# Optimization experiments

Hardware: AMD Instinct MI355X
Metric: run time of the kernel (lower is better)

Reference implementation:

```python
import jax, jax.numpy as jnp
import numpy as np

N = 5000      # nodes per event (hardcoded in PFNet7.forward)
BIN = 100     # LSH bin_size
K = 16        # kNN per node within bin
SLOPE = 0.01  # LeakyReLU default negative slope


def _mlp(x, W1, b1, W2, b2, W3, b3):
    h = jax.nn.leaky_relu(x @ W1 + b1, SLOPE)
    h = jax.nn.leaky_relu(h @ W2 + b2, SLOPE)
    return h @ W3 + b3


def _build_graph_lsh(x, codebook):
    # x: [N, F]. Faithful vectorized version of GraphBuildingLSH (batch=1).
    n_bins = N // BIN                                   # 50
    mul = x @ codebook[:, : n_bins // 2]                # [N, 25]
    cmul = jnp.concatenate([mul, -mul], axis=-1)        # [N, 50]
    bin_idx = jnp.argmax(cmul, axis=-1)                 # [N]
    bins_split = jnp.argsort(bin_idx).reshape(n_bins, BIN)  # [nb, BIN]
    pts = x[bins_split]                                 # [nb, BIN, F]
    dm = jax.nn.sigmoid(jnp.einsum('pif,pjf->pij', pts, pts))  # [nb, BIN, BIN]
    vals, inds = jax.lax.top_k(dm, K)                   # [nb, BIN, K]
    src = jnp.broadcast_to(bins_split[:, :, None], inds.shape).reshape(-1)
    dst = jnp.take_along_axis(bins_split, inds.reshape(n_bins, -1), axis=1).reshape(-1)
    val = vals.reshape(-1)                              # [nb*BIN*K] = 80000 edges
    return src, dst, val


def _gcn_conv(x, W, b, src, dst, ew):
    # PyG GCNConv: add self-loops (weight 1), symmetric normalization, aggregate at col.
    n = x.shape[0]
    loop = jnp.arange(n)
    row = jnp.concatenate([src, loop])
    col = jnp.concatenate([dst, loop])
    w = jnp.concatenate([ew, jnp.ones((n,), x.dtype)])
    deg = jax.ops.segment_sum(w, col, num_segments=n)
    dis = jnp.where(deg > 0, deg ** -0.5, 0.0)
    norm = dis[row] * w * dis[col]
    h = x @ W
    out = jax.ops.segment_sum(norm[:, None] * h[row], col, num_segments=n)
    return out + b


def _graph_conv(x, Wrel, brel, Wroot, src, dst, ew):
    # PyG GraphConv(aggr='add'): lin_rel(sum_j w_ij x_j) + lin_root(x)
    agg = jax.ops.segment_sum(ew[:, None] * x[src], dst, num_segments=x.shape[0])
    return agg @ Wrel + brel + x @ Wroot


def setup_inputs() -> dict:
    key = jax.random.key(0)
    ks = jax.random.split(key, 24)
    f32 = jnp.float32
    d = {
        'x': jax.random.normal(ks[0], (N, 12), f32),
        'ygen_id': jax.random.normal(ks[1], (N, 6), f32),
        'ygen': jax.random.normal(ks[2], (N, 6), f32),
        'codebook': jax.random.normal(ks[3], (12, 100), f32),
        # nn1: 12 -> 125 -> 125 -> 12
        'nn1_W1': jax.random.normal(ks[4], (12, 125), f32) * 0.1,
        'nn1_b1': jnp.zeros((125,), f32),
        'nn1_W2': jax.random.normal(ks[5], (125, 125), f32) * 0.1,
        'nn1_b2': jnp.zeros((125,), f32),
        'nn1_W3': jax.random.normal(ks[6], (125, 12), f32) * 0.1,
        'nn1_b3': jnp.zeros((12,), f32),
        # GCNConv: 12 -> 32
        'gcn_W': jax.random.normal(ks[7], (12, 32), f32) * 0.1,
        'gcn_b': jnp.zeros((32,), f32),
        # GraphConv: 32 -> 32
        'gc_Wrel': jax.random.normal(ks[8], (32, 32), f32) * 0.1,
        'gc_brel': jnp.zeros((32,), f32),
        'gc_Wroot': jax.random.normal(ks[9], (32, 32), f32) * 0.1,
        # nn2: 32 -> 125 -> 125 -> 6
        'nn2_W1': jax.random.normal(ks[10], (32, 125), f32) * 0.1,
        'nn2_b1': jnp.zeros((125,), f32),
        'nn2_W2': jax.random.normal(ks[11], (125, 125), f32) * 0.1,
        'nn2_b2': jnp.zeros((125,), f32),
        'nn2_W3': jax.random.normal(ks[12], (125, 6), f32) * 0.1,
        'nn2_b3': jnp.zeros((6,), f32),
        # nn3: 38 -> 125 -> 125 -> 6
        'nn3_W1': jax.random.normal(ks[13], (38, 125), f32) * 0.1,
        'nn3_b1': jnp.zeros((125,), f32),
        'nn3_W2': jax.random.normal(ks[14], (125, 125), f32) * 0.1,
        'nn3_b2': jnp.zeros((125,), f32),
        'nn3_W3': jax.random.normal(ks[15], (125, 6), f32) * 0.1,
        'nn3_b3': jnp.zeros((6,), f32),
    }
    return d


def reference(x, ygen_id, ygen, codebook,
              nn1_W1, nn1_b1, nn1_W2, nn1_b2, nn1_W3, nn1_b3,
              gcn_W, gcn_b, gc_Wrel, gc_brel, gc_Wroot,
              nn2_W1, nn2_b1, nn2_W2, nn2_b2, nn2_W3, nn2_b3,
              nn3_W1, nn3_b1, nn3_W2, nn3_b2, nn3_W3, nn3_b3):
    h = _mlp(x, nn1_W1, nn1_b1, nn1_W2, nn1_b2, nn1_W3, nn1_b3)   # [N, 12]
    src, dst, ew = _build_graph_lsh(h, codebook)
    h = jax.nn.leaky_relu(h, SLOPE)
    h = _gcn_conv(h, gcn_W, gcn_b, src, dst, ew)                   # [N, 32]
    h = _graph_conv(h, gc_Wrel, gc_brel, gc_Wroot, src, dst, ew)
    h = jax.nn.leaky_relu(h, SLOPE)
    cand_ids = _mlp(h, nn2_W1, nn2_b1, nn2_W2, nn2_b2, nn2_W3, nn2_b3)
    cand_p4 = _mlp(jnp.concatenate([h, cand_ids], axis=-1),
                   nn3_W1, nn3_b1, nn3_W2, nn3_b2, nn3_W3, nn3_b3)
    return (cand_ids, cand_p4, ygen_id, ygen)
```

## Files before the change

### kernel.cpp

```cpp
#include <hip/hip_runtime.h>
#include <math.h>

#define NN 5000
#define NBINS 50
#define BINSZ 100
#define KNN 16
#define BPAD 104
#define MROWS 112
#define NB 20

typedef _Float16 half8 __attribute__((ext_vector_type(8)));

__device__ __forceinline__ float lrelu(float x){ return x >= 0.f ? x : 0.01f*x; }

__global__ __launch_bounds__(640) void nn1_kernel(
    const float* __restrict__ x,
    const float* __restrict__ W1, const float* __restrict__ b1,
    const float* __restrict__ W2, const float* __restrict__ b2,
    const float* __restrict__ W3, const float* __restrict__ b3,
    const float* __restrict__ cb,
    float* __restrict__ h_out, int* __restrict__ bin_idx) {
    __shared__ float sW[8000];
    __shared__ float bufX[12 * NB];
    __shared__ float bufA[125 * NB];
    __shared__ float bufB[125 * NB];
    __shared__ float sCB[300];
    int tid = threadIdx.x;
    int n0 = blockIdx.x * NB;
    int g = tid >> 7, j = tid & 127;
    float acc[4];
    float4 r0, r1; float rt = 0.f;

    if (tid < 60) {
        float4 v = ((const float4*)(x + n0 * 12))[tid];
        int e = tid * 4;
        bufX[(e % 12) * NB + (e / 12)] = v.x;
        bufX[((e + 1) % 12) * NB + ((e + 1) / 12)] = v.y;
        bufX[((e + 2) % 12) * NB + ((e + 2) / 12)] = v.z;
        bufX[((e + 3) % 12) * NB + ((e + 3) / 12)] = v.w;
    }
    if (tid < 300) { int k = tid / 25, c = tid - k * 25; sCB[tid] = cb[k * 100 + c]; }
    if (tid < 375) ((float4*)sW)[tid] = ((const float4*)W1)[tid];
    __syncthreads();

    if (j < 125) {
        float bj = b1[j];
        acc[0] = bj; acc[1] = bj; acc[2] = bj; acc[3] = bj;
        #pragma unroll
        for (int k = 0; k < 12; ++k) {
            float w = sW[k * 125 + j];
            float4 a = *(const float4*)&bufX[k * NB + g * 4];
            acc[0] += a.x * w; acc[1] += a.y * w; acc[2] += a.z * w; acc[3] += a.w * w;
        }
        #pragma unroll
        for (int n = 0; n < 4; ++n) bufA[j * NB + g * 4 + n] = lrelu(acc[n]);
    }
    r0 = (tid < 1000) ? ((const float4*)W2)[tid] : make_float4(0.f,0.f,0.f,0.f);
    r1 = (tid < 360)  ? ((const float4*)W2)[tid + 640] : make_float4(0.f,0.f,0.f,0.f);
    __syncthreads();
    if (tid < 1000) ((float4*)sW)[tid] = r0;
    if (tid < 360)  ((float4*)sW)[tid + 640] = r1;
    __syncthreads();

    if (j < 125) { float bj = b2[j]; acc[0] = bj; acc[1] = bj; acc[2] = bj; acc[3] = bj; }
    for (int c = 0; c < 4; ++c) {
        if (c < 3) {
            int base = (c + 1) * 1000, nf4 = (c + 1 < 3) ? 1000 : 906;
            r0 = (tid < nf4) ? ((const float4*)W2)[base + tid] : make_float4(0.f,0.f,0.f,0.f);
            r1 = (tid + 640 < nf4) ? ((const float4*)W2)[base + tid + 640] : make_float4(0.f,0.f,0.f,0.f);
            if (c + 1 == 3 && tid == 0) rt = W2[15624];
        }
        int nk = (c < 3) ? 32 : 29;
        const float* wbuf = sW + (c & 1) * 4000;
        if (j < 125) {
            const float* arow = &bufA[(c * 32) * NB + g * 4];
            for (int k = 0; k < nk; ++k) {
                float w = wbuf[k * 125 + j];
                float4 a = *(const float4*)&arow[k * NB];
                acc[0] += a.x * w; acc[1] += a.y * w; acc[2] += a.z * w; acc[3] += a.w * w;
            }
        }
        if (c < 3) {
            float* dst = sW + ((c + 1) & 1) * 4000;
            int nf4 = (c + 1 < 3) ? 1000 : 906;
            if (tid < nf4) ((float4*)dst)[tid] = r0;
            if (tid + 640 < nf4) ((float4*)dst)[tid + 640] = r1;
            if (c + 1 == 3 && tid == 0) dst[3624] = rt;
            __syncthreads();
        }
    }
    if (j < 125) {
        #pragma unroll
        for (int n = 0; n < 4; ++n) bufB[j * NB + g * 4 + n] = lrelu(acc[n]);
    }
    __syncthreads();
    if (tid < 375) ((float4*)sW)[tid] = ((const float4*)W3)[tid];
    __syncthreads();

    if (j < 48) {
        int jj = j % 12, s = j / 12;
        int k0 = s * 32, nk = (s < 3) ? 32 : 29;
        float ps[4] = {0.f, 0.f, 0.f, 0.f};
        for (int k = 0; k < nk; ++k) {
            float w = sW[(k0 + k) * 12 + jj];
            float4 a = *(const float4*)&bufB[(k0 + k) * NB + g * 4];
            ps[0] += a.x * w; ps[1] += a.y * w; ps[2] += a.z * w; ps[3] += a.w * w;
        }
        #pragma unroll
        for (int n = 0; n < 4; ++n) bufA[(s * 12 + jj) * NB + g * 4 + n] = ps[n];
    }
    __syncthreads();
    if (tid < 240) {
        int jj = tid / 20, n = tid % 20;
        float v = bufA[jj * NB + n] + bufA[(12 + jj) * NB + n]
                + bufA[(24 + jj) * NB + n] + bufA[(36 + jj) * NB + n] + b3[jj];
        h_out[(n0 + n) * 12 + jj] = v;
        bufB[jj * NB + n] = v;
    }
    __syncthreads();

    if (tid < NB) {
        int n = tid;
        float hv[12];
        #pragma unroll
        for (int k = 0; k < 12; ++k) hv[k] = bufB[k * NB + n];
        float best = -INFINITY; int bi = 0;
        for (int c = 0; c < 25; ++c) {
            float m = 0.f;
            #pragma unroll
            for (int k = 0; k < 12; ++k) m += hv[k] * sCB[k * 25 + c];
            if (m > best) { best = m; bi = c; }
        }
        for (int c = 0; c < 25; ++c) {
            float m = 0.f;
            #pragma unroll
            for (int k = 0; k < 12; ++k) m += hv[k] * sCB[k * 25 + c];
            if (-m > best) { best = -m; bi = c + 25; }
        }
        bin_idx[n0 + n] = bi;
    }
}

__global__ __launch_bounds__(64) void scatter_kernel(
    const int* __restrict__ bin_idx, int* __restrict__ order) {
    __shared__ int sBI[NN];
    int b = blockIdx.x, lane = threadIdx.x;
    for (int t = lane; t < NN / 4; t += 64) ((int4*)sBI)[t] = ((const int4*)bin_idx)[t];
    __syncthreads();
    unsigned long long below = (lane == 0) ? 0ULL : ((~0ULL) >> (64 - lane));
    int cnt_lt = 0;
    for (int base = 0; base < NN; base += 64) {
        int i = base + lane;
        int bi = (i < NN) ? sBI[i] : 999;
        cnt_lt += __popcll(__ballot(bi < b));
    }
    int offs = cnt_lt;
    for (int base = 0; base < NN; base += 64) {
        int i = base + lane;
        int bi = (i < NN) ? sBI[i] : 999;
        unsigned long long m = __ballot(bi == b);
        if (bi == b) order[offs + __popcll(m & below)] = i;
        offs += __popcll(m);
    }
}

__global__ __launch_bounds__(256) void build_kernel(
    const float* __restrict__ h, const int* __restrict__ order,
    _Float16* __restrict__ Mg, float* __restrict__ dis_g) {
    __shared__ _Float16 M[BINSZ * BPAD];
    __shared__ float s_h[BINSZ * 12];
    __shared__ int   s_nodes[BINSZ];
    __shared__ unsigned s_tv[200 * KNN];
    int p = blockIdx.x, tid = threadIdx.x;

    if (tid < BINSZ) s_nodes[tid] = order[p * BINSZ + tid];
    for (int t = tid; t < BINSZ * BPAD / 2; t += 256) ((int*)M)[t] = 0;
    __syncthreads();
    for (int t = tid; t < BINSZ * 12; t += 256) {
        int i = t / 12, k = t - i * 12;
        s_h[t] = h[s_nodes[i] * 12 + k];
    }
    __syncthreads();

    if (tid < 200) {
        int row = tid >> 1, half = tid & 1;
        const float4* xp = (const float4*)&s_h[row * 12];
        float4 x0 = xp[0], x1 = xp[1], x2 = xp[2];
        unsigned tv[KNN];
        #pragma unroll
        for (int k = 0; k < KNN; ++k) tv[k] = 0u;
        int j0 = half * 50;
        for (int jj = 0; jj < 50; ++jj) {
            int j = j0 + jj;
            const float4* ap = (const float4*)&s_h[j * 12];
            float4 a0 = ap[0], a1 = ap[1], a2 = ap[2];
            float d = x0.x*a0.x + x0.y*a0.y + x0.z*a0.z + x0.w*a0.w
                    + x1.x*a1.x + x1.y*a1.y + x1.z*a1.z + x1.w*a1.w
                    + x2.x*a2.x + x2.y*a2.y + x2.z*a2.z + x2.w*a2.w;
            float v = 1.f / (1.f + expf(-d));
            unsigned key = (__float_as_uint(v) & 0xFFFFFF80u) | (unsigned)(127 - j);
            if (key > tv[KNN - 1]) {
                unsigned ins = key;
                #pragma unroll
                for (int k = 0; k < KNN; ++k) {
                    bool gt = ins > tv[k];
                    unsigned mx = gt ? ins : tv[k];
                    unsigned mn = gt ? tv[k] : ins;
                    tv[k] = mx; ins = mn;
                }
            }
        }
        #pragma unroll
        for (int k = 0; k < KNN; ++k) s_tv[tid * KNN + k] = tv[k];
    }
    __syncthreads();

    if (tid < BINSZ) {
        int base = tid * 32;
        int ia = 0, ib = 0;
        #pragma unroll
        for (int k = 0; k < KNN; ++k) {
            unsigned av = s_tv[base + ia], bv = s_tv[base + 16 + ib];
            bool tA = av > bv;
            unsigned key = tA ? av : bv;
            ia += tA; ib += !tA;
            int ix = 127 - (int)(key & 127u);
            float v = __uint_as_float(key & 0xFFFFFF80u);
            M[ix * BPAD + tid] = (_Float16)v;
        }
    }
    __syncthreads();

    for (int t = tid; t < BINSZ * BPAD / 8; t += 256)
        ((uint4*)(Mg + (size_t)p * BINSZ * BPAD))[t] = ((const uint4*)M)[t];
    if (tid < BINSZ) {
        float dsum = 1.0f;
        #pragma unroll 13
        for (int sc = 0; sc < 13; ++sc) {
            half8 m = *(const half8*)&M[tid * BPAD + sc * 8];
            dsum += (float)m[0] + (float)m[1] + (float)m[2] + (float)m[3]
                  + (float)m[4] + (float)m[5] + (float)m[6] + (float)m[7];
        }
        dis_g[p * BINSZ + tid] = 1.0f / sqrtf(dsum);
    }
}

__global__ __launch_bounds__(128) void conv_kernel(
    const _Float16* __restrict__ Mg, const float* __restrict__ dis_g,
    const float* __restrict__ h, const int* __restrict__ order,
    const float* __restrict__ gcn_W, const float* __restrict__ gcn_b,
    float* __restrict__ gcn_n, float* __restrict__ agg_n,
    const float4* __restrict__ ygen_id4, const float4* __restrict__ ygen4,
    float4* __restrict__ out4) {
    __shared__ _Float16 M[MROWS * BPAD];
    __shared__ float s_h[BINSZ * 12];
    __shared__ int   s_nodes[BINSZ];
    __shared__ float s_dis[BINSZ];
    __shared__ float s_w[12 * 8];
    __shared__ float s_hWd[8 * BPAD];
    __shared__ float s_gcn[8 * BPAD];
    int bid = blockIdx.x, tid = threadIdx.x;
    int p = bid >> 2, cg = bid & 3, c0 = cg * 8;

    if (tid < 75) {
        int gI = bid * 75 + tid;
        out4[15000 + gI] = (gI < 7500) ? ygen_id4[gI] : ygen4[gI - 7500];
    }
    if (tid < BINSZ) {
        s_nodes[tid] = order[p * BINSZ + tid];
        s_dis[tid]   = dis_g[p * BINSZ + tid];
    }
    for (int t = tid; t < 96; t += 128)
        s_w[t] = gcn_W[(t >> 3) * 32 + c0 + (t & 7)];
    for (int t = tid; t < BINSZ * BPAD / 8; t += 128)
        ((uint4*)M)[t] = ((const uint4*)(Mg + (size_t)p * BINSZ * BPAD))[t];
    for (int t = tid; t < (MROWS - BINSZ) * BPAD / 2; t += 128)
        ((int*)(M + BINSZ * BPAD))[t] = 0;
    if (tid < 32) {
        s_hWd[(tid >> 2) * BPAD + 100 + (tid & 3)] = 0.f;
        s_gcn[(tid >> 2) * BPAD + 100 + (tid & 3)] = 0.f;
    }
    __syncthreads();
    for (int t = tid; t < BINSZ * 12; t += 128) {
        int i = t / 12, k = t - i * 12;
        s_h[t] = h[s_nodes[i] * 12 + k];
    }
    __syncthreads();

    for (int o = tid; o < BINSZ * 8; o += 128) {
        int s = o >> 3, cc = o & 7;
        float a = 0.f;
        #pragma unroll
        for (int k = 0; k < 12; ++k) a += lrelu(s_h[s * 12 + k]) * s_w[k * 8 + cc];
        s_hWd[cc * BPAD + s] = s_dis[s] * a;
    }
    __syncthreads();

    int cc = tid & 7, dg = tid >> 3;
    {
        float acc[7];
        #pragma unroll
        for (int r = 0; r < 7; ++r) acc[r] = 0.f;
        for (int sc = 0; sc < 13; ++sc) {
            float4 hv0 = *(const float4*)&s_hWd[cc * BPAD + sc * 8];
            float4 hv1 = *(const float4*)&s_hWd[cc * BPAD + sc * 8 + 4];
            #pragma unroll
            for (int r = 0; r < 7; ++r) {
                int d = dg + 16 * r;
                half8 m = *(const half8*)&M[d * BPAD + sc * 8];
                acc[r] += (float)m[0]*hv0.x + (float)m[1]*hv0.y + (float)m[2]*hv0.z + (float)m[3]*hv0.w
                        + (float)m[4]*hv1.x + (float)m[5]*hv1.y + (float)m[6]*hv1.z + (float)m[7]*hv1.w;
            }
        }
        float bc = gcn_b[c0 + cc];
        #pragma unroll
        for (int r = 0; r < 7; ++r) {
            int d = dg + 16 * r;
            if (d < BINSZ) {
                float gq = s_dis[d] * (acc[r] + s_hWd[cc * BPAD + d]) + bc;
                s_gcn[cc * BPAD + d] = gq;
                gcn_n[s_nodes[d] * 32 + c0 + cc] = gq;
            }
        }
    }
    __syncthreads();
    {
        float acc[7];
        #pragma unroll
        for (int r = 0; r < 7; ++r) acc[r] = 0.f;
        for (int sc = 0; sc < 13; ++sc) {
            float4 hv0 = *(const float4*)&s_gcn[cc * BPAD + sc * 8];
            float4 hv1 = *(const float4*)&s_gcn[cc * BPAD + sc * 8 + 4];
            #pragma unroll
            for (int r = 0; r < 7; ++r) {
                int d = dg + 16 * r;
                half8 m = *(const half8*)&M[d * BPAD + sc * 8];
                acc[r] += (float)m[0]*hv0.x + (float)m[1]*hv0.y + (float)m[2]*hv0.z + (float)m[3]*hv0.w
                        + (float)m[4]*hv1.x + (float)m[5]*hv1.y + (float)m[6]*hv1.z + (float)m[7]*hv1.w;
            }
        }
        #pragma unroll
        for (int r = 0; r < 7; ++r) {
            int d = dg + 16 * r;
            if (d < BINSZ) agg_n[s_nodes[d] * 32 + c0 + cc] = acc[r];
        }
    }
}

__global__ __launch_bounds__(640) void nn23_kernel(
    const float* __restrict__ gcn_n, const float* __restrict__ agg_n,
    const float* __restrict__ Wrel, const float* __restrict__ brel,
    const float* __restrict__ Wroot,
    const float* __restrict__ A1, const float* __restrict__ ab1,
    const float* __restrict__ A2, const float* __restrict__ ab2,
    const float* __restrict__ A3, const float* __restrict__ ab3,
    const float* __restrict__ B1, const float* __restrict__ bb1,
    const float* __restrict__ B2, const float* __restrict__ bb2,
    const float* __restrict__ B3, const float* __restrict__ bb3,
    float* __restrict__ out_ids, float* __restrict__ out_p4) {
    __shared__ float sW[8000];
    __shared__ float sAG[32 * NB];
    __shared__ float sGC[32 * NB];
    __shared__ float bufC[38 * NB];
    __shared__ float bufA[125 * NB];
    __shared__ float bufB[125 * NB];
    int tid = threadIdx.x;
    int n0 = blockIdx.x * NB;
    int g = tid >> 7, j = tid & 127;
    float acc[4];
    float4 r0, r1; float rt = 0.f;

    if (tid < 160) {
        float4 va = ((const float4*)(agg_n + n0 * 32))[tid];
        float4 vg = ((const float4*)(gcn_n + n0 * 32))[tid];
        int e = tid * 4, n = e / 32, k = e % 32;
        sAG[k * NB + n] = va.x; sAG[(k+1) * NB + n] = va.y;
        sAG[(k+2) * NB + n] = va.z; sAG[(k+3) * NB + n] = va.w;
        sGC[k * NB + n] = vg.x; sGC[(k+1) * NB + n] = vg.y;
        sGC[(k+2) * NB + n] = vg.z; sGC[(k+3) * NB + n] = vg.w;
    }
    if (tid >= 160 && tid < 416) ((float4*)sW)[tid - 160] = ((const float4*)Wrel)[tid - 160];
    if (tid >= 416 && tid < 640) ((float4*)(sW + 1024))[tid - 416] = ((const float4*)Wroot)[tid - 416];
    if (tid < 32) ((float4*)(sW + 1024))[224 + tid] = ((const float4*)Wroot)[224 + tid];
    for (int t = tid; t < 1000; t += 640) ((float4*)(sW + 2048))[t] = ((const float4*)A1)[t];
    __syncthreads();

    {
        int jc = tid / 20, n = tid % 20;
        float a = brel[jc];
        #pragma unroll 8
        for (int k = 0; k < 32; ++k)
            a += sAG[k * NB + n] * sW[k * 32 + jc] + sGC[k * NB + n] * sW[1024 + k * 32 + jc];
        bufC[jc * NB + n] = lrelu(a);
    }
    __syncthreads();

    if (j < 125) {
        float bj = ab1[j];
        acc[0] = bj; acc[1] = bj; acc[2] = bj; acc[3] = bj;
        #pragma unroll 8
        for (int k = 0; k < 32; ++k) {
            float w = sW[2048 + k * 125 + j];
            float4 a = *(const float4*)&bufC[k * NB + g * 4];
            acc[0] += a.x * w; acc[1] += a.y * w; acc[2] += a.z * w; acc[3] += a.w * w;
        }
        #pragma unroll
        for (int n = 0; n < 4; ++n) bufA[j * NB + g * 4 + n] = lrelu(acc[n]);
    }
    r0 = (tid < 1000) ? ((const float4*)A2)[tid] : make_float4(0.f,0.f,0.f,0.f);
    r1 = (tid < 360)  ? ((const float4*)A2)[tid + 640] : make_float4(0.f,0.f,0.f,0.f);
    __syncthreads();
    if (tid < 1000) ((float4*)sW)[tid] = r0;
    if (tid < 360)  ((float4*)sW)[tid + 640] = r1;
    __syncthreads();

    if (j < 125) { float bj = ab2[j]; acc[0] = bj; acc[1] = bj; acc[2] = bj; acc[3] = bj; }
    for (int c = 0; c < 4; ++c) {
        if (c < 3) {
            int base = (c + 1) * 1000, nf4 = (c + 1 < 3) ? 1000 : 906;
            r0 = (tid < nf4) ? ((const float4*)A2)[base + tid] : make_float4(0.f,0.f,0.f,0.f);
            r1 = (tid + 640 < nf4) ? ((const float4*)A2)[base + tid + 640] : make_float4(0.f,0.f,0.f,0.f);
            if (c + 1 == 3 && tid == 0) rt = A2[15624];
        }
        int nk = (c < 3) ? 32 : 29;
        const float* wbuf = sW + (c & 1) * 4000;
        if (j < 125) {
            const float* arow = &bufA[(c * 32) * NB + g * 4];
            for (int k = 0; k < nk; ++k) {
                float w = wbuf[k * 125 + j];
                float4 a = *(const float4*)&arow[k * NB];
                acc[0] += a.x * w; acc[1] += a.y * w; acc[2] += a.z * w; acc[3] += a.w * w;
            }
        }
        if (c < 3) {
            float* dst = sW + ((c + 1) & 1) * 4000;
            int nf4 = (c + 1 < 3) ? 1000 : 906;
            if (tid < nf4) ((float4*)dst)[tid] = r0;
            if (tid + 640 < nf4) ((float4*)dst)[tid + 640] = r1;
            if (c + 1 == 3 && tid == 0) dst[3624] = rt;
            __syncthreads();
        }
    }
    if (j < 125) {
        #pragma unroll
        for (int n = 0; n < 4; ++n) bufB[j * NB + g * 4 + n] = lrelu(acc[n]);
    }
    __syncthreads();
    if (tid < 187) ((float4*)sW)[tid] = ((const float4*)A3)[tid];
    if (tid == 187) { sW[748] = A3[748]; sW[749] = A3[749]; }
    for (int t = tid; t < 1187; t += 640) ((float4*)(sW + 752))[t] = ((const float4*)B1)[t];
    if (tid == 188) { sW[752 + 4748] = B1[4748]; sW[752 + 4749] = B1[4749]; }
    __syncthreads();

    if (j < 24) {
        int jj = j % 6, s = j / 6;
        int k0 = s * 32, nk = (s < 3) ? 32 : 29;
        float ps[4] = {0.f, 0.f, 0.f, 0.f};
        for (int k = 0; k < nk; ++k) {
            float w = sW[(k0 + k) * 6 + jj];
            float4 a = *(const float4*)&bufB[(k0 + k) * NB + g * 4];
            ps[0] += a.x * w; ps[1] += a.y * w; ps[2] += a.z * w; ps[3] += a.w * w;
        }
        #pragma unroll
        for (int n = 0; n < 4; ++n) bufA[(s * 6 + jj) * NB + g * 4 + n] = ps[n];
    }
    __syncthreads();
    if (tid < 120) {
        int jj = tid / 20, n = tid % 20;
        float v = bufA[jj * NB + n] + bufA[(6 + jj) * NB + n]
                + bufA[(12 + jj) * NB + n] + bufA[(18 + jj) * NB + n] + ab3[jj];
        out_ids[(n0 + n) * 6 + jj] = v;
        bufC[(32 + jj) * NB + n] = v;
    }
    __syncthreads();

    if (j < 125) {
        float bj = bb1[j];
        acc[0] = bj; acc[1] = bj; acc[2] = bj; acc[3] = bj;
        #pragma unroll 2
        for (int k = 0; k < 38; ++k) {
            float w = sW[752 + k * 125 + j];
            float4 a = *(const float4*)&bufC[k * NB + g * 4];
            acc[0] += a.x * w; acc[1] += a.y * w; acc[2] += a.z * w; acc[3] += a.w * w;
        }
        #pragma unroll
        for (int n = 0; n < 4; ++n) bufA[j * NB + g * 4 + n] = lrelu(acc[n]);
    }
    r0 = (tid < 1000) ? ((const float4*)B2)[tid] : make_float4(0.f,0.f,0.f,0.f);
    r1 = (tid < 360)  ? ((const float4*)B2)[tid + 640] : make_float4(0.f,0.f,0.f,0.f);
    __syncthreads();
    if (tid < 1000) ((float4*)sW)[tid] = r0;
    if (tid < 360)  ((float4*)sW)[tid + 640] = r1;
    __syncthreads();

    if (j < 125) { float bj = bb2[j]; acc[0] = bj; acc[1] = bj; acc[2] = bj; acc[3] = bj; }
    for (int c = 0; c < 4; ++c) {
        if (c < 3) {
            int base = (c + 1) * 1000, nf4 = (c + 1 < 3) ? 1000 : 906;
            r0 = (tid < nf4) ? ((const float4*)B2)[base + tid] : make_float4(0.f,0.f,0.f,0.f);
            r1 = (tid + 640 < nf4) ? ((const float4*)B2)[base + tid + 640] : make_float4(0.f,0.f,0.f,0.f);
            if (c + 1 == 3 && tid == 0) rt = B2[15624];
        }
        int nk = (c < 3) ? 32 : 29;
        const float* wbuf = sW + (c & 1) * 4000;
        if (j < 125) {
            const float* arow = &bufA[(c * 32) * NB + g * 4];
            for (int k = 0; k < nk; ++k) {
                float w = wbuf[k * 125 + j];
                float4 a = *(const float4*)&arow[k * NB];
                acc[0] += a.x * w; acc[1] += a.y * w; acc[2] += a.z * w; acc[3] += a.w * w;
            }
        }
        if (c < 3) {
            float* dst = sW + ((c + 1) & 1) * 4000;
            int nf4 = (c + 1 < 3) ? 1000 : 906;
            if (tid < nf4) ((float4*)dst)[tid] = r0;
            if (tid + 640 < nf4) ((float4*)dst)[tid + 640] = r1;
            if (c + 1 == 3 && tid == 0) dst[3624] = rt;
            __syncthreads();
        }
    }
    if (j < 125) {
        #pragma unroll
        for (int n = 0; n < 4; ++n) bufB[j * NB + g * 4 + n] = lrelu(acc[n]);
    }
    __syncthreads();
    if (tid < 187) ((float4*)sW)[tid] = ((const float4*)B3)[tid];
    if (tid == 187) { sW[748] = B3[748]; sW[749] = B3[749]; }
    __syncthreads();

    if (j < 24) {
        int jj = j % 6, s = j / 6;
        int k0 = s * 32, nk = (s < 3) ? 32 : 29;
        float ps[4] = {0.f, 0.f, 0.f, 0.f};
        for (int k = 0; k < nk; ++k) {
            float w = sW[(k0 + k) * 6 + jj];
            float4 a = *(const float4*)&bufB[(k0 + k) * NB + g * 4];
            ps[0] += a.x * w; ps[1] += a.y * w; ps[2] += a.z * w; ps[3] += a.w * w;
        }
        #pragma unroll
        for (int n = 0; n < 4; ++n) bufA[(s * 6 + jj) * NB + g * 4 + n] = ps[n];
    }
    __syncthreads();
    if (tid < 120) {
        int jj = tid / 20, n = tid % 20;
        float v = bufA[jj * NB + n] + bufA[(6 + jj) * NB + n]
                + bufA[(12 + jj) * NB + n] + bufA[(18 + jj) * NB + n] + bb3[jj];
        out_p4[(n0 + n) * 6 + jj] = v;
    }
}

static inline int cdiv(int a, int b) { return (a + b - 1) / b; }

extern "C" void kernel_launch(void* const* d_in, const int* in_sizes, int n_in,
                              void* d_out, int out_size, void* d_ws, size_t ws_size,
                              hipStream_t stream) {
    const float* x        = (const float*)d_in[0];
    const float* ygen_id  = (const float*)d_in[1];
    const float* ygen     = (const float*)d_in[2];
    const float* codebook = (const float*)d_in[3];
    const float* nn1_W1 = (const float*)d_in[4];  const float* nn1_b1 = (const float*)d_in[5];
    const float* nn1_W2 = (const float*)d_in[6];  const float* nn1_b2 = (const float*)d_in[7];
    const float* nn1_W3 = (const float*)d_in[8];  const float* nn1_b3 = (const float*)d_in[9];
    const float* gcn_W  = (const float*)d_in[10]; const float* gcn_b  = (const float*)d_in[11];
    const float* gc_Wrel = (const float*)d_in[12]; const float* gc_brel = (const float*)d_in[13];
    const float* gc_Wroot = (const float*)d_in[14];
    const float* nn2_W1 = (const float*)d_in[15]; const float* nn2_b1 = (const float*)d_in[16];
    const float* nn2_W2 = (const float*)d_in[17]; const float* nn2_b2 = (const float*)d_in[18];
    const float* nn2_W3 = (const float*)d_in[19]; const float* nn2_b3 = (const float*)d_in[20];
    const float* nn3_W1 = (const float*)d_in[21]; const float* nn3_b1 = (const float*)d_in[22];
    const float* nn3_W2 = (const float*)d_in[23]; const float* nn3_b2 = (const float*)d_in[24];
    const float* nn3_W3 = (const float*)d_in[25]; const float* nn3_b3 = (const float*)d_in[26];

    float* out = (float*)d_out;
    float* ws  = (float*)d_ws;

    float* h      = ws + 0;
    float* gcn_n  = ws + 60000;
    float* agg_n  = ws + 220000;
    float* dis_g  = ws + 380000;
    _Float16* Mg  = (_Float16*)(ws + 385000);
    int* bin_idx  = (int*)(ws + 645000);
    int* order    = (int*)(ws + 650000);

    nn1_kernel<<<NN / NB, 640, 0, stream>>>(
        x, nn1_W1, nn1_b1, nn1_W2, nn1_b2, nn1_W3, nn1_b3, codebook,
        h, bin_idx);

    scatter_kernel<<<NBINS, 64, 0, stream>>>(bin_idx, order);

    build_kernel<<<NBINS, 256, 0, stream>>>(h, order, Mg, dis_g);

    conv_kernel<<<NBINS * 4, 128, 0, stream>>>(
        Mg, dis_g, h, order, gcn_W, gcn_b, gcn_n, agg_n,
        (const float4*)ygen_id, (const float4*)ygen, (float4*)out);

    nn23_kernel<<<NN / NB, 640, 0, stream>>>(
        gcn_n, agg_n, gc_Wrel, gc_brel, gc_Wroot,
        nn2_W1, nn2_b1, nn2_W2, nn2_b2, nn2_W3, nn2_b3,
        nn3_W1, nn3_b1, nn3_W2, nn3_b2, nn3_W3, nn3_b3,
        out, out + 30000);
}
```

Before: 198.6 us.

## Fuse all stages into one persistent kernel with global atomic barriers

Replaces the five separate launches (nn1, scatter, build, conv, nn23) with one persistent 250-block kernel. Stages are separated by a software grid barrier built from atomic counters, and each stage reuses a shared-memory union. The bin build and convolution are done per bin inside the same kernel, so the fp16 adjacency matrix no longer round-trips through global memory. This removes launch gaps and intermediate traffic, but it depends on all 250 blocks of 640 threads being co-resident, otherwise the barrier deadlocks. Most blocks sit idle during the 50-bin stages.

```diff
diff --git a/kernel.cpp b/kernel.cpp
--- a/kernel.cpp
+++ b/kernel.cpp
@@ -8,347 +8,70 @@
 #define BPAD 104
 #define MROWS 112
 #define NB 20
+#define NBLK 250
 
 typedef _Float16 half8 __attribute__((ext_vector_type(8)));
 
 __device__ __forceinline__ float lrelu(float x){ return x >= 0.f ? x : 0.01f*x; }
 
-__global__ __launch_bounds__(640) void nn1_kernel(
+union SharedU {
+    struct {
+        float sW[8000];
+        float bufX[12 * NB];
+        float bufA[125 * NB];
+        float bufB[125 * NB];
+        float sCB[300];
+    } p0;
+    struct {
+        int sBI[NN];
+        int s_lt[10];
+        int s_eq[10];
+    } p1;
+    struct {
+        _Float16 M[MROWS * BPAD];
+        float s_h[BINSZ * 12];
+        int   s_nodes[BINSZ];
+        float s_dis[BINSZ];
+        float s_w[12 * 32];
+        union {
+            unsigned s_tv[200 * KNN];
+            struct { float hWd[32 * BPAD]; float gcn[32 * BPAD]; } c;
+        } u;
+    } p2;
+    struct {
+        float sW[8000];
+        float sAG[32 * NB];
+        float sGC[32 * NB];
+        float bufC[38 * NB];
+        float bufA[125 * NB];
+        float bufB[125 * NB];
+    } p3;
+};
+
+__device__ __forceinline__ void gbar(int* bar, int idx) {
+    __syncthreads();
+    if (threadIdx.x == 0) {
+        __threadfence();
+        __hip_atomic_fetch_add(bar + idx, 1, __ATOMIC_RELEASE, __HIP_MEMORY_SCOPE_AGENT);
+        while (__hip_atomic_load(bar + idx, __ATOMIC_ACQUIRE, __HIP_MEMORY_SCOPE_AGENT) < NBLK)
+            __builtin_amdgcn_s_sleep(1);
+        __threadfence();
+    }
+    __syncthreads();
+}
+
+__global__ void init_kernel(int* bar) {
+    if (threadIdx.x < 8) bar[threadIdx.x] = 0;
+}
+
+__global__ __launch_bounds__(640) void fused_kernel(
     const float* __restrict__ x,
+    const float4* __restrict__ ygen_id4, const float4* __restrict__ ygen4,
+    const float* __restrict__ cb,
     const float* __restrict__ W1, const float* __restrict__ b1,
     const float* __restrict__ W2, const float* __restrict__ b2,
     const float* __restrict__ W3, const float* __restrict__ b3,
-    const float* __restrict__ cb,
-    float* __restrict__ h_out, int* __restrict__ bin_idx) {
-    __shared__ float sW[8000];
-    __shared__ float bufX[12 * NB];
-    __shared__ float bufA[125 * NB];
-    __shared__ float bufB[125 * NB];
-    __shared__ float sCB[300];
-    int tid = threadIdx.x;
-    int n0 = blockIdx.x * NB;
-    int g = tid >> 7, j = tid & 127;
-    float acc[4];
-    float4 r0, r1; float rt = 0.f;
-
-    if (tid < 60) {
-        float4 v = ((const float4*)(x + n0 * 12))[tid];
-        int e = tid * 4;
-        bufX[(e % 12) * NB + (e / 12)] = v.x;
-        bufX[((e + 1) % 12) * NB + ((e + 1) / 12)] = v.y;
-        bufX[((e + 2) % 12) * NB + ((e + 2) / 12)] = v.z;
-        bufX[((e + 3) % 12) * NB + ((e + 3) / 12)] = v.w;
-    }
-    if (tid < 300) { int k = tid / 25, c = tid - k * 25; sCB[tid] = cb[k * 100 + c]; }
-    if (tid < 375) ((float4*)sW)[tid] = ((const float4*)W1)[tid];
-    __syncthreads();
-
-    if (j < 125) {
-        float bj = b1[j];
-        acc[0] = bj; acc[1] = bj; acc[2] = bj; acc[3] = bj;
-        #pragma unroll
-        for (int k = 0; k < 12; ++k) {
-            float w = sW[k * 125 + j];
-            float4 a = *(const float4*)&bufX[k * NB + g * 4];
-            acc[0] += a.x * w; acc[1] += a.y * w; acc[2] += a.z * w; acc[3] += a.w * w;
-        }
-        #pragma unroll
-        for (int n = 0; n < 4; ++n) bufA[j * NB + g * 4 + n] = lrelu(acc[n]);
-    }
-    r0 = (tid < 1000) ? ((const float4*)W2)[tid] : make_float4(0.f,0.f,0.f,0.f);
-    r1 = (tid < 360)  ? ((const float4*)W2)[tid + 640] : make_float4(0.f,0.f,0.f,0.f);
-    __syncthreads();
-    if (tid < 1000) ((float4*)sW)[tid] = r0;
-    if (tid < 360)  ((float4*)sW)[tid + 640] = r1;
-    __syncthreads();
-
-    if (j < 125) { float bj = b2[j]; acc[0] = bj; acc[1] = bj; acc[2] = bj; acc[3] = bj; }
-    for (int c = 0; c < 4; ++c) {
-        if (c < 3) {
-            int base = (c + 1) * 1000, nf4 = (c + 1 < 3) ? 1000 : 906;
-            r0 = (tid < nf4) ? ((const float4*)W2)[base + tid] : make_float4(0.f,0.f,0.f,0.f);
-            r1 = (tid + 640 < nf4) ? ((const float4*)W2)[base + tid + 640] : make_float4(0.f,0.f,0.f,0.f);
-            if (c + 1 == 3 && tid == 0) rt = W2[15624];
-        }
-        int nk = (c < 3) ? 32 : 29;
-        const float* wbuf = sW + (c & 1) * 4000;
-        if (j < 125) {
-            const float* arow = &bufA[(c * 32) * NB + g * 4];
-            for (int k = 0; k < nk; ++k) {
-                float w = wbuf[k * 125 + j];
-                float4 a = *(const float4*)&arow[k * NB];
-                acc[0] += a.x * w; acc[1] += a.y * w; acc[2] += a.z * w; acc[3] += a.w * w;
-            }
-        }
-        if (c < 3) {
-            float* dst = sW + ((c + 1) & 1) * 4000;
-            int nf4 = (c + 1 < 3) ? 1000 : 906;
-            if (tid < nf4) ((float4*)dst)[tid] = r0;
-            if (tid + 640 < nf4) ((float4*)dst)[tid + 640] = r1;
-            if (c + 1 == 3 && tid == 0) dst[3624] = rt;
-            __syncthreads();
-        }
-    }
-    if (j < 125) {
-        #pragma unroll
-        for (int n = 0; n < 4; ++n) bufB[j * NB + g * 4 + n] = lrelu(acc[n]);
-    }
-    __syncthreads();
-    if (tid < 375) ((float4*)sW)[tid] = ((const float4*)W3)[tid];
-    __syncthreads();
-
-    if (j < 48) {
-        int jj = j % 12, s = j / 12;
-        int k0 = s * 32, nk = (s < 3) ? 32 : 29;
-        float ps[4] = {0.f, 0.f, 0.f, 0.f};
-        for (int k = 0; k < nk; ++k) {
-            float w = sW[(k0 + k) * 12 + jj];
-            float4 a = *(const float4*)&bufB[(k0 + k) * NB + g * 4];
-            ps[0] += a.x * w; ps[1] += a.y * w; ps[2] += a.z * w; ps[3] += a.w * w;
-        }
-        #pragma unroll
-        for (int n = 0; n < 4; ++n) bufA[(s * 12 + jj) * NB + g * 4 + n] = ps[n];
-    }
-    __syncthreads();
-    if (tid < 240) {
-        int jj = tid / 20, n = tid % 20;
-        float v = bufA[jj * NB + n] + bufA[(12 + jj) * NB + n]
-                + bufA[(24 + jj) * NB + n] + bufA[(36 + jj) * NB + n] + b3[jj];
-        h_out[(n0 + n) * 12 + jj] = v;
-        bufB[jj * NB + n] = v;
-    }
-    __syncthreads();
-
-    if (tid < NB) {
-        int n = tid;
-        float hv[12];
-        #pragma unroll
-        for (int k = 0; k < 12; ++k) hv[k] = bufB[k * NB + n];
-        float best = -INFINITY; int bi = 0;
-        for (int c = 0; c < 25; ++c) {
-            float m = 0.f;
-            #pragma unroll
-            for (int k = 0; k < 12; ++k) m += hv[k] * sCB[k * 25 + c];
-            if (m > best) { best = m; bi = c; }
-        }
-        for (int c = 0; c < 25; ++c) {
-            float m = 0.f;
-            #pragma unroll
-            for (int k = 0; k < 12; ++k) m += hv[k] * sCB[k * 25 + c];
-            if (-m > best) { best = -m; bi = c + 25; }
-        }
-        bin_idx[n0 + n] = bi;
-    }
-}
-
-__global__ __launch_bounds__(64) void scatter_kernel(
-    const int* __restrict__ bin_idx, int* __restrict__ order) {
-    __shared__ int sBI[NN];
-    int b = blockIdx.x, lane = threadIdx.x;
-    for (int t = lane; t < NN / 4; t += 64) ((int4*)sBI)[t] = ((const int4*)bin_idx)[t];
-    __syncthreads();
-    unsigned long long below = (lane == 0) ? 0ULL : ((~0ULL) >> (64 - lane));
-    int cnt_lt = 0;
-    for (int base = 0; base < NN; base += 64) {
-        int i = base + lane;
-        int bi = (i < NN) ? sBI[i] : 999;
-        cnt_lt += __popcll(__ballot(bi < b));
-    }
-    int offs = cnt_lt;
-    for (int base = 0; base < NN; base += 64) {
-        int i = base + lane;
-        int bi = (i < NN) ? sBI[i] : 999;
-        unsigned long long m = __ballot(bi == b);
-        if (bi == b) order[offs + __popcll(m & below)] = i;
-        offs += __popcll(m);
-    }
-}
-
-__global__ __launch_bounds__(256) void build_kernel(
-    const float* __restrict__ h, const int* __restrict__ order,
-    _Float16* __restrict__ Mg, float* __restrict__ dis_g) {
-    __shared__ _Float16 M[BINSZ * BPAD];
-    __shared__ float s_h[BINSZ * 12];
-    __shared__ int   s_nodes[BINSZ];
-    __shared__ unsigned s_tv[200 * KNN];
-    int p = blockIdx.x, tid = threadIdx.x;
-
-    if (tid < BINSZ) s_nodes[tid] = order[p * BINSZ + tid];
-    for (int t = tid; t < BINSZ * BPAD / 2; t += 256) ((int*)M)[t] = 0;
-    __syncthreads();
-    for (int t = tid; t < BINSZ * 12; t += 256) {
-        int i = t / 12, k = t - i * 12;
-        s_h[t] = h[s_nodes[i] * 12 + k];
-    }
-    __syncthreads();
-
-    if (tid < 200) {
-        int row = tid >> 1, half = tid & 1;
-        const float4* xp = (const float4*)&s_h[row * 12];
-        float4 x0 = xp[0], x1 = xp[1], x2 = xp[2];
-        unsigned tv[KNN];
-        #pragma unroll
-        for (int k = 0; k < KNN; ++k) tv[k] = 0u;
-        int j0 = half * 50;
-        for (int jj = 0; jj < 50; ++jj) {
-            int j = j0 + jj;
-            const float4* ap = (const float4*)&s_h[j * 12];
-            float4 a0 = ap[0], a1 = ap[1], a2 = ap[2];
-            float d = x0.x*a0.x + x0.y*a0.y + x0.z*a0.z + x0.w*a0.w
-                    + x1.x*a1.x + x1.y*a1.y + x1.z*a1.z + x1.w*a1.w
-                    + x2.x*a2.x + x2.y*a2.y + x2.z*a2.z + x2.w*a2.w;
-            float v = 1.f / (1.f + expf(-d));
-            unsigned key = (__float_as_uint(v) & 0xFFFFFF80u) | (unsigned)(127 - j);
-            if (key > tv[KNN - 1]) {
-                unsigned ins = key;
-                #pragma unroll
-                for (int k = 0; k < KNN; ++k) {
-                    bool gt = ins > tv[k];
-                    unsigned mx = gt ? ins : tv[k];
-                    unsigned mn = gt ? tv[k] : ins;
-                    tv[k] = mx; ins = mn;
-                }
-            }
-        }
-        #pragma unroll
-        for (int k = 0; k < KNN; ++k) s_tv[tid * KNN + k] = tv[k];
-    }
-    __syncthreads();
-
-    if (tid < BINSZ) {
-        int base = tid * 32;
-        int ia = 0, ib = 0;
-        #pragma unroll
-        for (int k = 0; k < KNN; ++k) {
-            unsigned av = s_tv[base + ia], bv = s_tv[base + 16 + ib];
-            bool tA = av > bv;
-            unsigned key = tA ? av : bv;
-            ia += tA; ib += !tA;
-            int ix = 127 - (int)(key & 127u);
-            float v = __uint_as_float(key & 0xFFFFFF80u);
-            M[ix * BPAD + tid] = (_Float16)v;
-        }
-    }
-    __syncthreads();
-
-    for (int t = tid; t < BINSZ * BPAD / 8; t += 256)
-        ((uint4*)(Mg + (size_t)p * BINSZ * BPAD))[t] = ((const uint4*)M)[t];
-    if (tid < BINSZ) {
-        float dsum = 1.0f;
-        #pragma unroll 13
-        for (int sc = 0; sc < 13; ++sc) {
-            half8 m = *(const half8*)&M[tid * BPAD + sc * 8];
-            dsum += (float)m[0] + (float)m[1] + (float)m[2] + (float)m[3]
-                  + (float)m[4] + (float)m[5] + (float)m[6] + (float)m[7];
-        }
-        dis_g[p * BINSZ + tid] = 1.0f / sqrtf(dsum);
-    }
-}
-
-__global__ __launch_bounds__(128) void conv_kernel(
-    const _Float16* __restrict__ Mg, const float* __restrict__ dis_g,
-    const float* __restrict__ h, const int* __restrict__ order,
     const float* __restrict__ gcn_W, const float* __restrict__ gcn_b,
-    float* __restrict__ gcn_n, float* __restrict__ agg_n,
-    const float4* __restrict__ ygen_id4, const float4* __restrict__ ygen4,
-    float4* __restrict__ out4) {
-    __shared__ _Float16 M[MROWS * BPAD];
-    __shared__ float s_h[BINSZ * 12];
-    __shared__ int   s_nodes[BINSZ];
-    __shared__ float s_dis[BINSZ];
-    __shared__ float s_w[12 * 8];
-    __shared__ float s_hWd[8 * BPAD];
-    __shared__ float s_gcn[8 * BPAD];
-    int bid = blockIdx.x, tid = threadIdx.x;
-    int p = bid >> 2, cg = bid & 3, c0 = cg * 8;
-
-    if (tid < 75) {
-        int gI = bid * 75 + tid;
-        out4[15000 + gI] = (gI < 7500) ? ygen_id4[gI] : ygen4[gI - 7500];
-    }
-    if (tid < BINSZ) {
-        s_nodes[tid] = order[p * BINSZ + tid];
-        s_dis[tid]   = dis_g[p * BINSZ + tid];
-    }
-    for (int t = tid; t < 96; t += 128)
-        s_w[t] = gcn_W[(t >> 3) * 32 + c0 + (t & 7)];
-    for (int t = tid; t < BINSZ * BPAD / 8; t += 128)
-        ((uint4*)M)[t] = ((const uint4*)(Mg + (size_t)p * BINSZ * BPAD))[t];
-    for (int t = tid; t < (MROWS - BINSZ) * BPAD / 2; t += 128)
-        ((int*)(M + BINSZ * BPAD))[t] = 0;
-    if (tid < 32) {
-        s_hWd[(tid >> 2) * BPAD + 100 + (tid & 3)] = 0.f;
-        s_gcn[(tid >> 2) * BPAD + 100 + (tid & 3)] = 0.f;
-    }
-    __syncthreads();
-    for (int t = tid; t < BINSZ * 12; t += 128) {
-        int i = t / 12, k = t - i * 12;
-        s_h[t] = h[s_nodes[i] * 12 + k];
-    }
-    __syncthreads();
-
-    for (int o = tid; o < BINSZ * 8; o += 128) {
-        int s = o >> 3, cc = o & 7;
-        float a = 0.f;
-        #pragma unroll
-        for (int k = 0; k < 12; ++k) a += lrelu(s_h[s * 12 + k]) * s_w[k * 8 + cc];
-        s_hWd[cc * BPAD + s] = s_dis[s] * a;
-    }
-    __syncthreads();
-
-    int cc = tid & 7, dg = tid >> 3;
-    {
-        float acc[7];
-        #pragma unroll
-        for (int r = 0; r < 7; ++r) acc[r] = 0.f;
-        for (int sc = 0; sc < 13; ++sc) {
-            float4 hv0 = *(const float4*)&s_hWd[cc * BPAD + sc * 8];
-            float4 hv1 = *(const float4*)&s_hWd[cc * BPAD + sc * 8 + 4];
-            #pragma unroll
-            for (int r = 0; r < 7; ++r) {
-                int d = dg + 16 * r;
-                half8 m = *(const half8*)&M[d * BPAD + sc * 8];
-                acc[r] += (float)m[0]*hv0.x + (float)m[1]*hv0.y + (float)m[2]*hv0.z + (float)m[3]*hv0.w
-                        + (float)m[4]*hv1.x + (float)m[5]*hv1.y + (float)m[6]*hv1.z + (float)m[7]*hv1.w;
-            }
-        }
-        float bc = gcn_b[c0 + cc];
-        #pragma unroll
-        for (int r = 0; r < 7; ++r) {
-            int d = dg + 16 * r;
-            if (d < BINSZ) {
-                float gq = s_dis[d] * (acc[r] + s_hWd[cc * BPAD + d]) + bc;
-                s_gcn[cc * BPAD + d] = gq;
-                gcn_n[s_nodes[d] * 32 + c0 + cc] = gq;
-            }
-        }
-    }
-    __syncthreads();
-    {
-        float acc[7];
-        #pragma unroll
-        for (int r = 0; r < 7; ++r) acc[r] = 0.f;
-        for (int sc = 0; sc < 13; ++sc) {
-            float4 hv0 = *(const float4*)&s_gcn[cc * BPAD + sc * 8];
-            float4 hv1 = *(const float4*)&s_gcn[cc * BPAD + sc * 8 + 4];
-            #pragma unroll
-            for (int r = 0; r < 7; ++r) {
-                int d = dg + 16 * r;
-                half8 m = *(const half8*)&M[d * BPAD + sc * 8];
-                acc[r] += (float)m[0]*hv0.x + (float)m[1]*hv0.y + (float)m[2]*hv0.z + (float)m[3]*hv0.w
-                        + (float)m[4]*hv1.x + (float)m[5]*hv1.y + (float)m[6]*hv1.z + (float)m[7]*hv1.w;
-            }
-        }
-        #pragma unroll
-        for (int r = 0; r < 7; ++r) {
-            int d = dg + 16 * r;
-            if (d < BINSZ) agg_n[s_nodes[d] * 32 + c0 + cc] = acc[r];
-        }
-    }
-}
-
-__global__ __launch_bounds__(640) void nn23_kernel(
-    const float* __restrict__ gcn_n, const float* __restrict__ agg_n,
     const float* __restrict__ Wrel, const float* __restrict__ brel,
     const float* __restrict__ Wroot,
     const float* __restrict__ A1, const float* __restrict__ ab1,
@@ -357,200 +80,495 @@
     const float* __restrict__ B1, const float* __restrict__ bb1,
     const float* __restrict__ B2, const float* __restrict__ bb2,
     const float* __restrict__ B3, const float* __restrict__ bb3,
-    float* __restrict__ out_ids, float* __restrict__ out_p4) {
-    __shared__ float sW[8000];
-    __shared__ float sAG[32 * NB];
-    __shared__ float sGC[32 * NB];
-    __shared__ float bufC[38 * NB];
-    __shared__ float bufA[125 * NB];
-    __shared__ float bufB[125 * NB];
+    float* __restrict__ h, float* __restrict__ gcn_n, float* __restrict__ agg_n,
+    int* __restrict__ bin_idx, int* __restrict__ order, int* __restrict__ bar,
+    float* __restrict__ out_ids, float* __restrict__ out_p4,
+    float4* __restrict__ out4)
+{
+    __shared__ SharedU S;
     int tid = threadIdx.x;
-    int n0 = blockIdx.x * NB;
-    int g = tid >> 7, j = tid & 127;
-    float acc[4];
-    float4 r0, r1; float rt = 0.f;
-
-    if (tid < 160) {
-        float4 va = ((const float4*)(agg_n + n0 * 32))[tid];
-        float4 vg = ((const float4*)(gcn_n + n0 * 32))[tid];
-        int e = tid * 4, n = e / 32, k = e % 32;
-        sAG[k * NB + n] = va.x; sAG[(k+1) * NB + n] = va.y;
-        sAG[(k+2) * NB + n] = va.z; sAG[(k+3) * NB + n] = va.w;
-        sGC[k * NB + n] = vg.x; sGC[(k+1) * NB + n] = vg.y;
-        sGC[(k+2) * NB + n] = vg.z; sGC[(k+3) * NB + n] = vg.w;
+
+    {
+        int n0 = blockIdx.x * NB;
+        int g = tid >> 7, j = tid & 127;
+        float acc[4];
+        float4 r0, r1; float rt = 0.f;
+
+        if (tid < 60) {
+            float4 v = ((const float4*)(x + n0 * 12))[tid];
+            int e = tid * 4;
+            S.p0.bufX[(e % 12) * NB + (e / 12)] = v.x;
+            S.p0.bufX[((e + 1) % 12) * NB + ((e + 1) / 12)] = v.y;
+            S.p0.bufX[((e + 2) % 12) * NB + ((e + 2) / 12)] = v.z;
+            S.p0.bufX[((e + 3) % 12) * NB + ((e + 3) / 12)] = v.w;
+        }
+        if (tid < 300) { int k = tid / 25, c = tid - k * 25; S.p0.sCB[tid] = cb[k * 100 + c]; }
+        if (tid < 375) ((float4*)S.p0.sW)[tid] = ((const float4*)W1)[tid];
+        __syncthreads();
+
+        if (j < 125) {
+            float bj = b1[j];
+            acc[0] = bj; acc[1] = bj; acc[2] = bj; acc[3] = bj;
+            #pragma unroll
+            for (int k = 0; k < 12; ++k) {
+                float w = S.p0.sW[k * 125 + j];
+                float4 a = *(const float4*)&S.p0.bufX[k * NB + g * 4];
+                acc[0] += a.x * w; acc[1] += a.y * w; acc[2] += a.z * w; acc[3] += a.w * w;
+            }
+            #pragma unroll
+            for (int n = 0; n < 4; ++n) S.p0.bufA[j * NB + g * 4 + n] = lrelu(acc[n]);
+        }
+        r0 = (tid < 1000) ? ((const float4*)W2)[tid] : make_float4(0.f,0.f,0.f,0.f);
+        r1 = (tid < 360)  ? ((const float4*)W2)[tid + 640] : make_float4(0.f,0.f,0.f,0.f);
+        __syncthreads();
+        if (tid < 1000) ((float4*)S.p0.sW)[tid] = r0;
+        if (tid < 360)  ((float4*)S.p0.sW)[tid + 640] = r1;
+        __syncthreads();
+
+        if (j < 125) { float bj = b2[j]; acc[0] = bj; acc[1] = bj; acc[2] = bj; acc[3] = bj; }
+        for (int c = 0; c < 4; ++c) {
+            if (c < 3) {
+                int base = (c + 1) * 1000, nf4 = (c + 1 < 3) ? 1000 : 906;
+                r0 = (tid < nf4) ? ((const float4*)W2)[base + tid] : make_float4(0.f,0.f,0.f,0.f);
+                r1 = (tid + 640 < nf4) ? ((const float4*)W2)[base + tid + 640] : make_float4(0.f,0.f,0.f,0.f);
+                if (c + 1 == 3 && tid == 0) rt = W2[15624];
+            }
+            int nk = (c < 3) ? 32 : 29;
+            const float* wbuf = S.p0.sW + (c & 1) * 4000;
+            if (j < 125) {
+                const float* arow = &S.p0.bufA[(c * 32) * NB + g * 4];
+                for (int k = 0; k < nk; ++k) {
+                    float w = wbuf[k * 125 + j];
+                    float4 a = *(const float4*)&arow[k * NB];
+                    acc[0] += a.x * w; acc[1] += a.y * w; acc[2] += a.z * w; acc[3] += a.w * w;
+                }
+            }
+            if (c < 3) {
+                float* dst = S.p0.sW + ((c + 1) & 1) * 4000;
+                int nf4 = (c + 1 < 3) ? 1000 : 906;
+                if (tid < nf4) ((float4*)dst)[tid] = r0;
+                if (tid + 640 < nf4) ((float4*)dst)[tid + 640] = r1;
+                if (c + 1 == 3 && tid == 0) dst[3624] = rt;
+                __syncthreads();
+            }
+        }
+        if (j < 125) {
+            #pragma unroll
+            for (int n = 0; n < 4; ++n) S.p0.bufB[j * NB + g * 4 + n] = lrelu(acc[n]);
+        }
+        __syncthreads();
+        if (tid < 375) ((float4*)S.p0.sW)[tid] = ((const float4*)W3)[tid];
+        __syncthreads();
+
+        if (j < 48) {
+            int jj = j % 12, s = j / 12;
+            int k0 = s * 32, nk = (s < 3) ? 32 : 29;
+            float ps[4] = {0.f, 0.f, 0.f, 0.f};
+            for (int k = 0; k < nk; ++k) {
+                float w = S.p0.sW[(k0 + k) * 12 + jj];
+                float4 a = *(const float4*)&S.p0.bufB[(k0 + k) * NB + g * 4];
+                ps[0] += a.x * w; ps[1] += a.y * w; ps[2] += a.z * w; ps[3] += a.w * w;
+            }
+            #pragma unroll
+            for (int n = 0; n < 4; ++n) S.p0.bufA[(s * 12 + jj) * NB + g * 4 + n] = ps[n];
+        }
+        __syncthreads();
+        if (tid < 240) {
+            int jj = tid / 20, n = tid % 20;
+            float v = S.p0.bufA[jj * NB + n] + S.p0.bufA[(12 + jj) * NB + n]
+                    + S.p0.bufA[(24 + jj) * NB + n] + S.p0.bufA[(36 + jj) * NB + n] + b3[jj];
+            h[(n0 + n) * 12 + jj] = v;
+            S.p0.bufB[jj * NB + n] = v;
+        }
+        __syncthreads();
+
+        if (tid < NB) {
+            int n = tid;
+            float hv[12];
+            #pragma unroll
+            for (int k = 0; k < 12; ++k) hv[k] = S.p0.bufB[k * NB + n];
+            float best = -INFINITY; int bi = 0;
+            for (int c = 0; c < 25; ++c) {
+                float m = 0.f;
+                #pragma unroll
+                for (int k = 0; k < 12; ++k) m += hv[k] * S.p0.sCB[k * 25 + c];
+                if (m > best) { best = m; bi = c; }
+            }
+            for (int c = 0; c < 25; ++c) {
+                float m = 0.f;
+                #pragma unroll
+                for (int k = 0; k < 12; ++k) m += hv[k] * S.p0.sCB[k * 25 + c];
+                if (-m > best) { best = -m; bi = c + 25; }
+            }
+            bin_idx[n0 + n] = bi;
+        }
     }
-    if (tid >= 160 && tid < 416) ((float4*)sW)[tid - 160] = ((const float4*)Wrel)[tid - 160];
-    if (tid >= 416 && tid < 640) ((float4*)(sW + 1024))[tid - 416] = ((const float4*)Wroot)[tid - 416];
-    if (tid < 32) ((float4*)(sW + 1024))[224 + tid] = ((const float4*)Wroot)[224 + tid];
-    for (int t = tid; t < 1000; t += 640) ((float4*)(sW + 2048))[t] = ((const float4*)A1)[t];
-    __syncthreads();
+    gbar(bar, 0);
+
+    if (blockIdx.x < NBINS) {
+        int bb = blockIdx.x;
+        for (int t = tid; t < NN / 4; t += 640) ((int4*)S.p1.sBI)[t] = ((const int4*)bin_idx)[t];
+        __syncthreads();
+        int lane = tid & 63, w = tid >> 6;
+        int start = w * 512;
+        int end = (start + 512 > NN) ? NN : start + 512;
+        int cnt_lt = 0, cnt_eq = 0;
+        for (int base = start; base < end; base += 64) {
+            int i = base + lane;
+            int bi = (i < end) ? S.p1.sBI[i] : 999;
+            cnt_lt += __popcll(__ballot(bi < bb));
+            cnt_eq += __popcll(__ballot(bi == bb));
+        }
+        if (lane == 0) { S.p1.s_lt[w] = cnt_lt; S.p1.s_eq[w] = cnt_eq; }
+        __syncthreads();
+        int offs = 0;
+        #pragma unroll
+        for (int w2 = 0; w2 < 10; ++w2) {
+            offs += S.p1.s_lt[w2];
+            if (w2 < w) offs += S.p1.s_eq[w2];
+        }
+        unsigned long long below = lane ? ((~0ULL) >> (64 - lane)) : 0ULL;
+        for (int base = start; base < end; base += 64) {
+            int i = base + lane;
+            int bi = (i < end) ? S.p1.sBI[i] : 999;
+            unsigned long long m = __ballot(bi == bb);
+            if (bi == bb) order[offs + __popcll(m & below)] = i;
+            offs += __popcll(m);
+        }
+    } else {
+        if (tid < 75) {
+            int gI = ((int)blockIdx.x - NBINS) * 75 + tid;
+            out4[15000 + gI] = (gI < 7500) ? ygen_id4[gI] : ygen4[gI - 7500];
+        }
+    }
+    gbar(bar, 1);
+
+    if (blockIdx.x < NBINS) {
+        int p = blockIdx.x;
+        if (tid < BINSZ) S.p2.s_nodes[tid] = order[p * BINSZ + tid];
+        for (int t = tid; t < MROWS * BPAD / 2; t += 640) ((int*)S.p2.M)[t] = 0;
+        if (tid < 384) S.p2.s_w[tid] = gcn_W[tid];
+        __syncthreads();
+        for (int t = tid; t < BINSZ * 12; t += 640) {
+            int i = t / 12, k = t - i * 12;
+            S.p2.s_h[t] = h[S.p2.s_nodes[i] * 12 + k];
+        }
+        __syncthreads();
+
+        if (tid < 200) {
+            int row = tid >> 1, half = tid & 1;
+            const float4* xp = (const float4*)&S.p2.s_h[row * 12];
+            float4 x0 = xp[0], x1 = xp[1], x2 = xp[2];
+            unsigned tv[KNN];
+            #pragma unroll
+            for (int k = 0; k < KNN; ++k) tv[k] = 0u;
+            int j0 = half * 50;
+            for (int jj = 0; jj < 50; ++jj) {
+                int jn = j0 + jj;
+                const float4* ap = (const float4*)&S.p2.s_h[jn * 12];
+                float4 a0 = ap[0], a1 = ap[1], a2 = ap[2];
+                float d = x0.x*a0.x + x0.y*a0.y + x0.z*a0.z + x0.w*a0.w
+                        + x1.x*a1.x + x1.y*a1.y + x1.z*a1.z + x1.w*a1.w
+                        + x2.x*a2.x + x2.y*a2.y + x2.z*a2.z + x2.w*a2.w;
+                float v = 1.f / (1.f + expf(-d));
+                unsigned key = (__float_as_uint(v) & 0xFFFFFF80u) | (unsigned)(127 - jn);
+                if (key > tv[KNN - 1]) {
+                    unsigned ins = key;
+                    #pragma unroll
+                    for (int k = 0; k < KNN; ++k) {
+                        bool gt = ins > tv[k];
+                        unsigned mx = gt ? ins : tv[k];
+                        unsigned mn = gt ? tv[k] : ins;
+                        tv[k] = mx; ins = mn;
+                    }
+                }
+            }
+            #pragma unroll
+            for (int k = 0; k < KNN; ++k) S.p2.u.s_tv[tid * KNN + k] = tv[k];
+        }
+        __syncthreads();
+
+        if (tid < BINSZ) {
+            int mbase = tid * 32;
+            int ia = 0, ib = 0;
+            #pragma unroll
+            for (int k = 0; k < KNN; ++k) {
+                unsigned av = S.p2.u.s_tv[mbase + ia], bv = S.p2.u.s_tv[mbase + 16 + ib];
+                bool tA = av > bv;
+                unsigned key = tA ? av : bv;
+                ia += tA; ib += !tA;
+                int ix = 127 - (int)(key & 127u);
+                S.p2.M[ix * BPAD + tid] = (_Float16)__uint_as_float(key & 0xFFFFFF80u);
+            }
+        }
+        __syncthreads();
+        if (tid < BINSZ) {
+            float dsum = 1.0f;
+            #pragma unroll 13
+            for (int sc = 0; sc < 13; ++sc) {
+                half8 m = *(const half8*)&S.p2.M[tid * BPAD + sc * 8];
+                dsum += (float)m[0] + (float)m[1] + (float)m[2] + (float)m[3]
+                      + (float)m[4] + (float)m[5] + (float)m[6] + (float)m[7];
+            }
+            S.p2.s_dis[tid] = 1.0f / sqrtf(dsum);
+        }
+        __syncthreads();
+
+        if (tid < 256) {
+            int c = tid >> 3, r = tid & 7;
+            if (r < 4) S.p2.u.c.hWd[c * BPAD + 100 + r] = 0.f;
+            else       S.p2.u.c.gcn[c * BPAD + 100 + (r - 4)] = 0.f;
+        }
+        for (int o = tid; o < BINSZ * 32; o += 640) {
+            int s = o >> 5, c = o & 31;
+            float a = 0.f;
+            #pragma unroll
+            for (int k = 0; k < 12; ++k) a += lrelu(S.p2.s_h[s * 12 + k]) * S.p2.s_w[k * 32 + c];
+            S.p2.u.c.hWd[c * BPAD + s] = S.p2.s_dis[s] * a;
+        }
+        __syncthreads();
+
+        if (tid < 512) {
+            int cg = tid >> 7, t1 = tid & 127, cc = t1 & 7, dg = t1 >> 3;
+            int c = cg * 8 + cc;
+            float acc7[7];
+            #pragma unroll
+            for (int r = 0; r < 7; ++r) acc7[r] = 0.f;
+            for (int sc = 0; sc < 13; ++sc) {
+                float4 hv0 = *(const float4*)&S.p2.u.c.hWd[c * BPAD + sc * 8];
+                float4 hv1 = *(const float4*)&S.p2.u.c.hWd[c * BPAD + sc * 8 + 4];
+                #pragma unroll
+                for (int r = 0; r < 7; ++r) {
+                    int d = dg + 16 * r;
+                    half8 m = *(const half8*)&S.p2.M[d * BPAD + sc * 8];
+                    acc7[r] += (float)m[0]*hv0.x + (float)m[1]*hv0.y + (float)m[2]*hv0.z + (float)m[3]*hv0.w
+                             + (float)m[4]*hv1.x + (float)m[5]*hv1.y + (float)m[6]*hv1.z + (float)m[7]*hv1.w;
+                }
+            }
+            float bc = gcn_b[c];
+            #pragma unroll
+            for (int r = 0; r < 7; ++r) {
+                int d = dg + 16 * r;
+                if (d < BINSZ) {
+                    float gq = S.p2.s_dis[d] * (acc7[r] + S.p2.u.c.hWd[c * BPAD + d]) + bc;
+                    S.p2.u.c.gcn[c * BPAD + d] = gq;
+                    gcn_n[S.p2.s_nodes[d] * 32 + c] = gq;
+                }
+            }
+        }
+        __syncthreads();
+        if (tid < 512) {
+            int cg = tid >> 7, t1 = tid & 127, cc = t1 & 7, dg = t1 >> 3;
+            int c = cg * 8 + cc;
+            float acc7[7];
+            #pragma unroll
+            for (int r = 0; r < 7; ++r) acc7[r] = 0.f;
+            for (int sc = 0; sc < 13; ++sc) {
+                float4 hv0 = *(const float4*)&S.p2.u.c.gcn[c * BPAD + sc * 8];
+                float4 hv1 = *(const float4*)&S.p2.u.c.gcn[c * BPAD + sc * 8 + 4];
+                #pragma unroll
+                for (int r = 0; r < 7; ++r) {
+                    int d = dg + 16 * r;
+                    half8 m = *(const half8*)&S.p2.M[d * BPAD + sc * 8];
+                    acc7[r] += (float)m[0]*hv0.x + (float)m[1]*hv0.y + (float)m[2]*hv0.z + (float)m[3]*hv0.w
+                             + (float)m[4]*hv1.x + (float)m[5]*hv1.y + (float)m[6]*hv1.z + (float)m[7]*hv1.w;
+                }
+            }
+            #pragma unroll
+            for (int r = 0; r < 7; ++r) {
+                int d = dg + 16 * r;
+                if (d < BINSZ) agg_n[S.p2.s_nodes[d] * 32 + c] = acc7[r];
+            }
+        }
+    }
+    gbar(bar, 2);
 
     {
-        int jc = tid / 20, n = tid % 20;
-        float a = brel[jc];
-        #pragma unroll 8
-        for (int k = 0; k < 32; ++k)
-            a += sAG[k * NB + n] * sW[k * 32 + jc] + sGC[k * NB + n] * sW[1024 + k * 32 + jc];
-        bufC[jc * NB + n] = lrelu(a);
-    }
-    __syncthreads();
-
-    if (j < 125) {
-        float bj = ab1[j];
-        acc[0] = bj; acc[1] = bj; acc[2] = bj; acc[3] = bj;
-        #pragma unroll 8
-        for (int k = 0; k < 32; ++k) {
-            float w = sW[2048 + k * 125 + j];
-            float4 a = *(const float4*)&bufC[k * NB + g * 4];
-            acc[0] += a.x * w; acc[1] += a.y * w; acc[2] += a.z * w; acc[3] += a.w * w;
-        }
-        #pragma unroll
-        for (int n = 0; n < 4; ++n) bufA[j * NB + g * 4 + n] = lrelu(acc[n]);
-    }
-    r0 = (tid < 1000) ? ((const float4*)A2)[tid] : make_float4(0.f,0.f,0.f,0.f);
-    r1 = (tid < 360)  ? ((const float4*)A2)[tid + 640] : make_float4(0.f,0.f,0.f,0.f);
-    __syncthreads();
-    if (tid < 1000) ((float4*)sW)[tid] = r0;
-    if (tid < 360)  ((float4*)sW)[tid + 640] = r1;
-    __syncthreads();
-
-    if (j < 125) { float bj = ab2[j]; acc[0] = bj; acc[1] = bj; acc[2] = bj; acc[3] = bj; }
-    for (int c = 0; c < 4; ++c) {
-        if (c < 3) {
-            int base = (c + 1) * 1000, nf4 = (c + 1 < 3) ? 1000 : 906;
-            r0 = (tid < nf4) ? ((const float4*)A2)[base + tid] : make_float4(0.f,0.f,0.f,0.f);
-            r1 = (tid + 640 < nf4) ? ((const float4*)A2)[base + tid + 640] : make_float4(0.f,0.f,0.f,0.f);
-            if (c + 1 == 3 && tid == 0) rt = A2[15624];
-        }
-        int nk = (c < 3) ? 32 : 29;
-        const float* wbuf = sW + (c & 1) * 4000;
+        int n0 = blockIdx.x * NB;
+        int g = tid >> 7, j = tid & 127;
+        float acc[4];
+        float4 r0, r1; float rt = 0.f;
+
+        if (tid < 160) {
+            float4 va = ((const float4*)(agg_n + n0 * 32))[tid];
+            float4 vg = ((const float4*)(gcn_n + n0 * 32))[tid];
+            int e = tid * 4, n = e / 32, k = e % 32;
+            S.p3.sAG[k * NB + n] = va.x; S.p3.sAG[(k+1) * NB + n] = va.y;
+            S.p3.sAG[(k+2) * NB + n] = va.z; S.p3.sAG[(k+3) * NB + n] = va.w;
+            S.p3.sGC[k * NB + n] = vg.x; S.p3.sGC[(k+1) * NB + n] = vg.y;
+            S.p3.sGC[(k+2) * NB + n] = vg.z; S.p3.sGC[(k+3) * NB + n] = vg.w;
+        }
+        if (tid >= 160 && tid < 416) ((float4*)S.p3.sW)[tid - 160] = ((const float4*)Wrel)[tid - 160];
+        if (tid >= 416 && tid < 640) ((float4*)(S.p3.sW + 1024))[tid - 416] = ((const float4*)Wroot)[tid - 416];
+        if (tid < 32) ((float4*)(S.p3.sW + 1024))[224 + tid] = ((const float4*)Wroot)[224 + tid];
+        for (int t = tid; t < 1000; t += 640) ((float4*)(S.p3.sW + 2048))[t] = ((const float4*)A1)[t];
+        __syncthreads();
+
+        {
+            int jc = tid / 20, n = tid % 20;
+            float a = brel[jc];
+            #pragma unroll 8
+            for (int k = 0; k < 32; ++k)
+                a += S.p3.sAG[k * NB + n] * S.p3.sW[k * 32 + jc] + S.p3.sGC[k * NB + n] * S.p3.sW[1024 + k * 32 + jc];
+            S.p3.bufC[jc * NB + n] = lrelu(a);
+        }
+        __syncthreads();
+
         if (j < 125) {
-            const float* arow = &bufA[(c * 32) * NB + g * 4];
+            float bj = ab1[j];
+            acc[0] = bj; acc[1] = bj; acc[2] = bj; acc[3] = bj;
+            #pragma unroll 8
+            for (int k = 0; k < 32; ++k) {
+                float w = S.p3.sW[2048 + k * 125 + j];
+                float4 a = *(const float4*)&S.p3.bufC[k * NB + g * 4];
+                acc[0] += a.x * w; acc[1] += a.y * w; acc[2] += a.z * w; acc[3] += a.w * w;
+            }
+            #pragma unroll
+            for (int n = 0; n < 4; ++n) S.p3.bufA[j * NB + g * 4 + n] = lrelu(acc[n]);
+        }
+        r0 = (tid < 1000) ? ((const float4*)A2)[tid] : make_float4(0.f,0.f,0.f,0.f);
+        r1 = (tid < 360)  ? ((const float4*)A2)[tid + 640] : make_float4(0.f,0.f,0.f,0.f);
+        __syncthreads();
+        if (tid < 1000) ((float4*)S.p3.sW)[tid] = r0;
+        if (tid < 360)  ((float4*)S.p3.sW)[tid + 640] = r1;
+        __syncthreads();
+
+        if (j < 125) { float bj = ab2[j]; acc[0] = bj; acc[1] = bj; acc[2] = bj; acc[3] = bj; }
+        for (int c = 0; c < 4; ++c) {
+            if (c < 3) {
+                int base = (c + 1) * 1000, nf4 = (c + 1 < 3) ? 1000 : 906;
+                r0 = (tid < nf4) ? ((const float4*)A2)[base + tid] : make_float4(0.f,0.f,0.f,0.f);
+                r1 = (tid + 640 < nf4) ? ((const float4*)A2)[base + tid + 640] : make_float4(0.f,0.f,0.f,0.f);
+                if (c + 1 == 3 && tid == 0) rt = A2[15624];
+            }
+            int nk = (c < 3) ? 32 : 29;
+            const float* wbuf = S.p3.sW + (c & 1) * 4000;
+            if (j < 125) {
+                const float* arow = &S.p3.bufA[(c * 32) * NB + g * 4];
+                for (int k = 0; k < nk; ++k) {
+                    float w = wbuf[k * 125 + j];
+                    float4 a = *(const float4*)&arow[k * NB];
+                    acc[0] += a.x * w; acc[1] += a.y * w; acc[2] += a.z * w; acc[3] += a.w * w;
+                }
+            }
+            if (c < 3) {
+                float* dst = S.p3.sW + ((c + 1) & 1) * 4000;
+                int nf4 = (c + 1 < 3) ? 1000 : 906;
+                if (tid < nf4) ((float4*)dst)[tid] = r0;
+                if (tid + 640 < nf4) ((float4*)dst)[tid + 640] = r1;
+                if (c + 1 == 3 && tid == 0) dst[3624] = rt;
+                __syncthreads();
+            }
+        }
+        if (j < 125) {
+            #pragma unroll
+            for (int n = 0; n < 4; ++n) S.p3.bufB[j * NB + g * 4 + n] = lrelu(acc[n]);
+        }
+        __syncthreads();
+        if (tid < 187) ((float4*)S.p3.sW)[tid] = ((const float4*)A3)[tid];
+        if (tid == 187) { S.p3.sW[748] = A3[748]; S.p3.sW[749] = A3[749]; }
+        for (int t = tid; t < 1187; t += 640) ((float4*)(S.p3.sW + 752))[t] = ((const float4*)B1)[t];
+        if (tid == 188) { S.p3.sW[752 + 4748] = B1[4748]; S.p3.sW[752 + 4749] = B1[4749]; }
+        __syncthreads();
+
+        if (j < 24) {
+            int jj = j % 6, s = j / 6;
+            int k0 = s * 32, nk = (s < 3) ? 32 : 29;
+            float ps[4] = {0.f, 0.f, 0.f, 0.f};
             for (int k = 0; k < nk; ++k) {
-                float w = wbuf[k * 125 + j];
-                float4 a = *(const float4*)&arow[k * NB];
+                float w = S.p3.sW[(k0 + k) * 6 + jj];
+                float4 a = *(const float4*)&S.p3.bufB[(k0 + k) * NB + g * 4];
+                ps[0] += a.x * w; ps[1] += a.y * w; ps[2] += a.z * w; ps[3] += a.w * w;
+            }
+            #pragma unroll
+            for (int n = 0; n < 4; ++n) S.p3.bufA[(s * 6 + jj) * NB + g * 4 + n] = ps[n];
+        }
+        __syncthreads();
+        if (tid < 120) {
+            int jj = tid / 20, n = tid % 20;
+            float v = S.p3.bufA[jj * NB + n] + S.p3.bufA[(6 + jj) * NB + n]
+                    + S.p3.bufA[(12 + jj) * NB + n] + S.p3.bufA[(18 + jj) * NB + n] + ab3[jj];
+            out_ids[(n0 + n) * 6 + jj] = v;
+            S.p3.bufC[(32 + jj) * NB + n] = v;
+        }
+        __syncthreads();
+
+        if (j < 125) {
+            float bj = bb1[j];
+            acc[0] = bj; acc[1] = bj; acc[2] = bj; acc[3] = bj;
+            #pragma unroll 2
+            for (int k = 0; k < 38; ++k) {
+                float w = S.p3.sW[752 + k * 125 + j];
+                float4 a = *(const float4*)&S.p3.bufC[k * NB + g * 4];
                 acc[0] += a.x * w; acc[1] += a.y * w; acc[2] += a.z * w; acc[3] += a.w * w;
             }
-        }
-        if (c < 3) {
-            float* dst = sW + ((c + 1) & 1) * 4000;
-            int nf4 = (c + 1 < 3) ? 1000 : 906;
-            if (tid < nf4) ((float4*)dst)[tid] = r0;
-            if (tid + 640 < nf4) ((float4*)dst)[tid + 640] = r1;
-            if (c + 1 == 3 && tid == 0) dst[3624] = rt;
-            __syncthreads();
-        }
-    }
-    if (j < 125) {
-        #pragma unroll
-        for (int n = 0; n < 4; ++n) bufB[j * NB + g * 4 + n] = lrelu(acc[n]);
-    }
-    __syncthreads();
-    if (tid < 187) ((float4*)sW)[tid] = ((const float4*)A3)[tid];
-    if (tid == 187) { sW[748] = A3[748]; sW[749] = A3[749]; }
-    for (int t = tid; t < 1187; t += 640) ((float4*)(sW + 752))[t] = ((const float4*)B1)[t];
-    if (tid == 188) { sW[752 + 4748] = B1[4748]; sW[752 + 4749] = B1[4749]; }
-    __syncthreads();
-
-    if (j < 24) {
-        int jj = j % 6, s = j / 6;
-        int k0 = s * 32, nk = (s < 3) ? 32 : 29;
-        float ps[4] = {0.f, 0.f, 0.f, 0.f};
-        for (int k = 0; k < nk; ++k) {
-            float w = sW[(k0 + k) * 6 + jj];
-            float4 a = *(const float4*)&bufB[(k0 + k) * NB + g * 4];
-            ps[0] += a.x * w; ps[1] += a.y * w; ps[2] += a.z * w; ps[3] += a.w * w;
-        }
-        #pragma unroll
-        for (int n = 0; n < 4; ++n) bufA[(s * 6 + jj) * NB + g * 4 + n] = ps[n];
-    }
-    __syncthreads();
-    if (tid < 120) {
-        int jj = tid / 20, n = tid % 20;
-        float v = bufA[jj * NB + n] + bufA[(6 + jj) * NB + n]
-                + bufA[(12 + jj) * NB + n] + bufA[(18 + jj) * NB + n] + ab3[jj];
-        out_ids[(n0 + n) * 6 + jj] = v;
-        bufC[(32 + jj) * NB + n] = v;
-    }
-    __syncthreads();
-
-    if (j < 125) {
-        float bj = bb1[j];
-        acc[0] = bj; acc[1] = bj; acc[2] = bj; acc[3] = bj;
-        #pragma unroll 2
-        for (int k = 0; k < 38; ++k) {
-            float w = sW[752 + k * 125 + j];
-            float4 a = *(const float4*)&bufC[k * NB + g * 4];
-            acc[0] += a.x * w; acc[1] += a.y * w; acc[2] += a.z * w; acc[3] += a.w * w;
-        }
-        #pragma unroll
-        for (int n = 0; n < 4; ++n) bufA[j * NB + g * 4 + n] = lrelu(acc[n]);
-    }
-    r0 = (tid < 1000) ? ((const float4*)B2)[tid] : make_float4(0.f,0.f,0.f,0.f);
-    r1 = (tid < 360)  ? ((const float4*)B2)[tid + 640] : make_float4(0.f,0.f,0.f,0.f);
-    __syncthreads();
-    if (tid < 1000) ((float4*)sW)[tid] = r0;
-    if (tid < 360)  ((float4*)sW)[tid + 640] = r1;
-    __syncthreads();
-
-    if (j < 125) { float bj = bb2[j]; acc[0] = bj; acc[1] = bj; acc[2] = bj; acc[3] = bj; }
-    for (int c = 0; c < 4; ++c) {
-        if (c < 3) {
-            int base = (c + 1) * 1000, nf4 = (c + 1 < 3) ? 1000 : 906;
-            r0 = (tid < nf4) ? ((const float4*)B2)[base + tid] : make_float4(0.f,0.f,0.f,0.f);
-            r1 = (tid + 640 < nf4) ? ((const float4*)B2)[base + tid + 640] : make_float4(0.f,0.f,0.f,0.f);
-            if (c + 1 == 3 && tid == 0) rt = B2[15624];
-        }
-        int nk = (c < 3) ? 32 : 29;
-        const float* wbuf = sW + (c & 1) * 4000;
+            #pragma unroll
+            for (int n = 0; n < 4; ++n) S.p3.bufA[j * NB + g * 4 + n] = lrelu(acc[n]);
+        }
+        r0 = (tid < 1000) ? ((const float4*)B2)[tid] : make_float4(0.f,0.f,0.f,0.f);
+        r1 = (tid < 360)  ? ((const float4*)B2)[tid + 640] : make_float4(0.f,0.f,0.f,0.f);
+        __syncthreads();
+        if (tid < 1000) ((float4*)S.p3.sW)[tid] = r0;
+        if (tid < 360)  ((float4*)S.p3.sW)[tid + 640] = r1;
+        __syncthreads();
+
+        if (j < 125) { float bj = bb2[j]; acc[0] = bj; acc[1] = bj; acc[2] = bj; acc[3] = bj; }
+        for (int c = 0; c < 4; ++c) {
+            if (c < 3) {
+                int base = (c + 1) * 1000, nf4 = (c + 1 < 3) ? 1000 : 906;
+                r0 = (tid < nf4) ? ((const float4*)B2)[base + tid] : make_float4(0.f,0.f,0.f,0.f);
+                r1 = (tid + 640 < nf4) ? ((const float4*)B2)[base + tid + 640] : make_float4(0.f,0.f,0.f,0.f);
+                if (c + 1 == 3 && tid == 0) rt = B2[15624];
+            }
+            int nk = (c < 3) ? 32 : 29;
+            const float* wbuf = S.p3.sW + (c & 1) * 4000;
+            if (j < 125) {
+                const float* arow = &S.p3.bufA[(c * 32) * NB + g * 4];
+                for (int k = 0; k < nk; ++k) {
+                    float w = wbuf[k * 125 + j];
+                    float4 a = *(const float4*)&arow[k * NB];
+                    acc[0] += a.x * w; acc[1] += a.y * w; acc[2] += a.z * w; acc[3] += a.w * w;
+                }
+            }
+            if (c < 3) {
+                float* dst = S.p3.sW + ((c + 1) & 1) * 4000;
+                int nf4 = (c + 1 < 3) ? 1000 : 906;
+                if (tid < nf4) ((float4*)dst)[tid] = r0;
+                if (tid + 640 < nf4) ((float4*)dst)[tid + 640] = r1;
+                if (c + 1 == 3 && tid == 0) dst[3624] = rt;
+                __syncthreads();
+            }
+        }
         if (j < 125) {
-            const float* arow = &bufA[(c * 32) * NB + g * 4];
+            #pragma unroll
+            for (int n = 0; n < 4; ++n) S.p3.bufB[j * NB + g * 4 + n] = lrelu(acc[n]);
+        }
+        __syncthreads();
+        if (tid < 187) ((float4*)S.p3.sW)[tid] = ((const float4*)B3)[tid];
+        if (tid == 187) { S.p3.sW[748] = B3[748]; S.p3.sW[749] = B3[749]; }
+        __syncthreads();
+
+        if (j < 24) {
+            int jj = j % 6, s = j / 6;
+            int k0 = s * 32, nk = (s < 3) ? 32 : 29;
+            float ps[4] = {0.f, 0.f, 0.f, 0.f};
             for (int k = 0; k < nk; ++k) {
-                float w = wbuf[k * 125 + j];
-                float4 a = *(const float4*)&arow[k * NB];
-                acc[0] += a.x * w; acc[1] += a.y * w; acc[2] += a.z * w; acc[3] += a.w * w;
-            }
-        }
-        if (c < 3) {
-            float* dst = sW + ((c + 1) & 1) * 4000;
-            int nf4 = (c + 1 < 3) ? 1000 : 906;
-            if (tid < nf4) ((float4*)dst)[tid] = r0;
-            if (tid + 640 < nf4) ((float4*)dst)[tid + 640] = r1;
-            if (c + 1 == 3 && tid == 0) dst[3624] = rt;
-            __syncthreads();
-        }
-    }
-    if (j < 125) {
-        #pragma unroll
-        for (int n = 0; n < 4; ++n) bufB[j * NB + g * 4 + n] = lrelu(acc[n]);
-    }
-    __syncthreads();
-    if (tid < 187) ((float4*)sW)[tid] = ((const float4*)B3)[tid];
-    if (tid == 187) { sW[748] = B3[748]; sW[749] = B3[749]; }
-    __syncthreads();
-
-    if (j < 24) {
-        int jj = j % 6, s = j / 6;
-        int k0 = s * 32, nk = (s < 3) ? 32 : 29;
-        float ps[4] = {0.f, 0.f, 0.f, 0.f};
-        for (int k = 0; k < nk; ++k) {
-            float w = sW[(k0 + k) * 6 + jj];
-            float4 a = *(const float4*)&bufB[(k0 + k) * NB + g * 4];
-            ps[0] += a.x * w; ps[1] += a.y * w; ps[2] += a.z * w; ps[3] += a.w * w;
-        }
-        #pragma unroll
-        for (int n = 0; n < 4; ++n) bufA[(s * 6 + jj) * NB + g * 4 + n] = ps[n];
-    }
-    __syncthreads();
-    if (tid < 120) {
-        int jj = tid / 20, n = tid % 20;
-        float v = bufA[jj * NB + n] + bufA[(6 + jj) * NB + n]
-                + bufA[(12 + jj) * NB + n] + bufA[(18 + jj) * NB + n] + bb3[jj];
-        out_p4[(n0 + n) * 6 + jj] = v;
+                float w = S.p3.sW[(k0 + k) * 6 + jj];
+                float4 a = *(const float4*)&S.p3.bufB[(k0 + k) * NB + g * 4];
+                ps[0] += a.x * w; ps[1] += a.y * w; ps[2] += a.z * w; ps[3] += a.w * w;
+            }
+            #pragma unroll
+            for (int n = 0; n < 4; ++n) S.p3.bufA[(s * 6 + jj) * NB + g * 4 + n] = ps[n];
+        }
+        __syncthreads();
+        if (tid < 120) {
+            int jj = tid / 20, n = tid % 20;
+            float v = S.p3.bufA[jj * NB + n] + S.p3.bufA[(6 + jj) * NB + n]
+                    + S.p3.bufA[(12 + jj) * NB + n] + S.p3.bufA[(18 + jj) * NB + n] + bb3[jj];
+            out_p4[(n0 + n) * 6 + jj] = v;
+        }
     }
 }
-
-static inline int cdiv(int a, int b) { return (a + b - 1) / b; }
 
 extern "C" void kernel_launch(void* const* d_in, const int* in_sizes, int n_in,
                               void* d_out, int out_size, void* d_ws, size_t ws_size,
@@ -578,26 +596,18 @@
     float* h      = ws + 0;
     float* gcn_n  = ws + 60000;
     float* agg_n  = ws + 220000;
-    float* dis_g  = ws + 380000;
-    _Float16* Mg  = (_Float16*)(ws + 385000);
-    int* bin_idx  = (int*)(ws + 645000);
-    int* order    = (int*)(ws + 650000);
-
-    nn1_kernel<<<NN / NB, 640, 0, stream>>>(
-        x, nn1_W1, nn1_b1, nn1_W2, nn1_b2, nn1_W3, nn1_b3, codebook,
-        h, bin_idx);
-
-    scatter_kernel<<<NBINS, 64, 0, stream>>>(bin_idx, order);
-
-    build_kernel<<<NBINS, 256, 0, stream>>>(h, order, Mg, dis_g);
-
-    conv_kernel<<<NBINS * 4, 128, 0, stream>>>(
-        Mg, dis_g, h, order, gcn_W, gcn_b, gcn_n, agg_n,
-        (const float4*)ygen_id, (const float4*)ygen, (float4*)out);
-
-    nn23_kernel<<<NN / NB, 640, 0, stream>>>(
-        gcn_n, agg_n, gc_Wrel, gc_brel, gc_Wroot,
+    int* bin_idx  = (int*)(ws + 380000);
+    int* order    = (int*)(ws + 385000);
+    int* bar      = (int*)(ws + 390000);
+
+    init_kernel<<<1, 64, 0, stream>>>(bar);
+
+    fused_kernel<<<NBLK, 640, 0, stream>>>(
+        x, (const float4*)ygen_id, (const float4*)ygen, codebook,
+        nn1_W1, nn1_b1, nn1_W2, nn1_b2, nn1_W3, nn1_b3,
+        gcn_W, gcn_b, gc_Wrel, gc_brel, gc_Wroot,
         nn2_W1, nn2_b1, nn2_W2, nn2_b2, nn2_W3, nn2_b3,
         nn3_W1, nn3_b1, nn3_W2, nn3_b2, nn3_W3, nn3_b3,
-        out, out + 30000);
+        h, gcn_n, agg_n, bin_idx, order, bar,
+        out, out + 30000, (float4*)out);
 }
```

Measured after the change: 242.8 us. 1.22x slower.
